# Optimization experiments

Measured on AMD Instinct MI355X. Metric: run time of the kernel, lower is better.

Reference implementation:

```python
import jax, jax.numpy as jnp
import numpy as np
from jax import lax

V, E, H, B, S = 50257, 512, 1024, 128, 256

def setup_inputs() -> dict:
    key = jax.random.key(0)
    k0, k1, k2, k3, k4, k5 = jax.random.split(key, 6)
    scale = 1.0 / np.sqrt(H)  # PyTorch LSTMCell init range ~ U(-1/sqrt(H), 1/sqrt(H))
    return {
        "inputs": jax.random.randint(k0, (B, S), 0, V),
        "embed_table": jax.random.normal(k1, (V, E), dtype=jnp.float32) * 0.02,
        "W_ih": jax.random.uniform(k2, (4 * H, E), dtype=jnp.float32, minval=-scale, maxval=scale),
        "W_hh": jax.random.uniform(k3, (4 * H, H), dtype=jnp.float32, minval=-scale, maxval=scale),
        "b_ih": jax.random.uniform(k4, (4 * H,), dtype=jnp.float32, minval=-scale, maxval=scale),
        "b_hh": jax.random.uniform(k5, (4 * H,), dtype=jnp.float32, minval=-scale, maxval=scale),
    }

def reference(inputs, embed_table, W_ih, W_hh, b_ih, b_hh):
    # Embedding lookup: [B, S, E]
    embeds = embed_table[inputs]
    bias = b_ih + b_hh  # [4H]

    def step(h, x_t):
        # x_t: [B, E], h: [B, H]
        gates = x_t @ W_ih.T + h @ W_hh.T + bias  # [B, 4H]
        i, f, g, o = jnp.split(gates, 4, axis=-1)  # PyTorch gate order: i, f, g, o
        # FAITHFUL to original bug: new cell state is discarded each step, so the
        # carried cell state is always zero -> c_t = sigmoid(i) * tanh(g).
        c_t = jax.nn.sigmoid(i) * jnp.tanh(g)
        h_new = jax.nn.sigmoid(o) * jnp.tanh(c_t)
        return h_new, None

    h0 = jnp.zeros((B, H), dtype=embeds.dtype)
    xs = jnp.swapaxes(embeds, 0, 1)  # [S, B, E]
    h_last, _ = lax.scan(step, h0, xs)
    return h_last  # [B, H]
```

## Files before the change

### kernel.cpp

```cpp
#include <hip/hip_runtime.h>
#include <hip/hip_fp16.h>


typedef __fp16 f16x8 __attribute__((ext_vector_type(8)));
typedef __fp16 f16x4 __attribute__((ext_vector_type(4)));
typedef float  f32x4 __attribute__((ext_vector_type(4)));

#define MFMA16(a, b, c) __builtin_amdgcn_mfma_f32_16x16x32_f16(a, b, c, 0, 0, 0)

__device__ __forceinline__ float sigmoid_f(float x) {
  return 1.f / (1.f + __expf(-x));
}
__device__ __forceinline__ float tanh_f(float x) {
  x = fminf(fmaxf(x, -15.f), 15.f);
  float e = __expf(2.f * x);
  return (e - 1.f) / (e + 1.f);
}

static constexpr int SS = 256;

__global__ void prep_kernel(const float* __restrict__ W_ih, const float* __restrict__ W_hh,
                            const float* __restrict__ b_ih, const float* __restrict__ b_hh,
                            __fp16* __restrict__ Wi3, __fp16* __restrict__ Wh3,
                            float* __restrict__ bias3) {
  int j3 = blockIdx.x;
  int g = j3 >> 10, j = j3 & 1023;
  int orig = (g == 0 ? 0 : (g == 1 ? 2048 : 3072)) + j;
  int tid = threadIdx.x;
  {
    float4 v = *(const float4*)(W_hh + (size_t)orig * 1024 + tid * 4);
    f16x4 o = {(__fp16)v.x, (__fp16)v.y, (__fp16)v.z, (__fp16)v.w};
    *(f16x4*)(Wh3 + (size_t)j3 * 1024 + tid * 4) = o;
  }
  if (tid < 128) {
    float4 v = *(const float4*)(W_ih + (size_t)orig * 512 + tid * 4);
    f16x4 o = {(__fp16)v.x, (__fp16)v.y, (__fp16)v.z, (__fp16)v.w};
    *(f16x4*)(Wi3 + (size_t)j3 * 512 + tid * 4) = o;
  }
  if (tid == 0) bias3[j3] = b_ih[orig] + b_hh[orig];
}

__global__ void gather_kernel(const int* __restrict__ tok, const float* __restrict__ emb,
                              __fp16* __restrict__ X) {
  int m = blockIdx.x;
  int t = m >> 7, b = m & 127;
  int tk = tok[b * SS + t];
  int e0 = threadIdx.x * 8;
  const float* src = emb + (size_t)tk * 512 + e0;
  float4 v0 = *(const float4*)src;
  float4 v1 = *(const float4*)(src + 4);
  f16x8 o;
  o[0] = (__fp16)v0.x; o[1] = (__fp16)v0.y; o[2] = (__fp16)v0.z; o[3] = (__fp16)v0.w;
  o[4] = (__fp16)v1.x; o[5] = (__fp16)v1.y; o[6] = (__fp16)v1.z; o[7] = (__fp16)v1.w;
  *(f16x8*)(X + (size_t)m * 512 + e0) = o;
}

__global__ __launch_bounds__(256, 1) void recur_kernel(const __fp16* __restrict__ Wh3,
                                                       const __fp16* __restrict__ Wi3,
                                                       const __fp16* __restrict__ X,
                                                       const float* __restrict__ bias3,
                                                       __fp16* __restrict__ hbuf,
                                                       int* __restrict__ cnt,
                                                       float* __restrict__ out) {
  const int bid = blockIdx.x;
  const int bg = bid & 7, n = bid >> 3;
  const int b0 = bg * 16, j0 = n * 32;
  const int tid = threadIdx.x, wid = tid >> 6, lane = tid & 63;
  const int l15 = lane & 15, quad = lane >> 4;
  const int kq = wid;
  const int ct_e = wid & 1, rh = wid >> 1;

  __shared__ float gbuf[2][4][3][2][16][20];

  f16x8 wh[3][2][8];
  f16x8 wi[3][2][4];
#pragma unroll
  for (int g = 0; g < 3; ++g)
#pragma unroll
    for (int ct = 0; ct < 2; ++ct) {
      const __fp16* wr = Wh3 + (size_t)(g * 1024 + j0 + ct * 16 + l15) * 1024 + kq * 256 + quad * 8;
#pragma unroll
      for (int kk = 0; kk < 8; ++kk) wh[g][ct][kk] = *(const f16x8*)(wr + kk * 32);
      const __fp16* wr2 = Wi3 + (size_t)(g * 1024 + j0 + ct * 16 + l15) * 512 + kq * 128 + quad * 8;
#pragma unroll
      for (int kk = 0; kk < 4; ++kk) wi[g][ct][kk] = *(const f16x8*)(wr2 + kk * 32);
    }

  float bs[3];
#pragma unroll
  for (int g = 0; g < 3; ++g) bs[g] = bias3[g * 1024 + j0 + ct_e * 16 + l15];

  const __fp16* xrow = X + (size_t)(b0 + l15) * 512 + kq * 128 + quad * 8;
  const __fp16* hrow = hbuf + (size_t)(b0 + l15) * 1024 + kq * 256 + quad * 8;
  int* cbase = cnt + (bg << 8) * 16;

  for (int t = 0; t < SS; ++t) {
    f16x8 xa[4];
    {
      const __fp16* xp = xrow + (size_t)t * 65536;
#pragma unroll
      for (int kk = 0; kk < 4; ++kk) xa[kk] = *(const f16x8*)(xp + kk * 32);
    }
    if (t > 0) {
      const int* pollp = cbase + t * 16;
      for (;;) {
        int v = __hip_atomic_load(pollp, __ATOMIC_RELAXED, __HIP_MEMORY_SCOPE_AGENT);
        if (v >= 32) break;
        __builtin_amdgcn_s_sleep(1);
      }
      asm volatile("" ::: "memory");
    }
    f16x8 ha[8];
    {
      const __fp16* hp = hrow + (size_t)t * 131072;
#pragma unroll
      for (int kk = 0; kk < 8; ++kk) ha[kk] = *(const f16x8*)(hp + kk * 32);
    }
    f32x4 acc[3][2];
#pragma unroll
    for (int g = 0; g < 3; ++g)
#pragma unroll
      for (int ct = 0; ct < 2; ++ct) {
        f32x4 z = {0.f, 0.f, 0.f, 0.f};
        acc[g][ct] = z;
      }
#pragma unroll
    for (int kk = 0; kk < 4; ++kk)
#pragma unroll
      for (int g = 0; g < 3; ++g)
#pragma unroll
        for (int ct = 0; ct < 2; ++ct)
          acc[g][ct] = MFMA16(xa[kk], wi[g][ct][kk], acc[g][ct]);
#pragma unroll
    for (int kk = 0; kk < 8; ++kk)
#pragma unroll
      for (int g = 0; g < 3; ++g)
#pragma unroll
        for (int ct = 0; ct < 2; ++ct)
          acc[g][ct] = MFMA16(ha[kk], wh[g][ct][kk], acc[g][ct]);
    const int tp = t & 1;
#pragma unroll
    for (int g = 0; g < 3; ++g)
#pragma unroll
      for (int ct = 0; ct < 2; ++ct)
#pragma unroll
        for (int r = 0; r < 4; ++r)
          gbuf[tp][kq][g][ct][quad * 4 + r][l15] = acc[g][ct][r];
    __syncthreads();
    float sum[3][2];
#pragma unroll
    for (int g = 0; g < 3; ++g)
#pragma unroll
      for (int rr = 0; rr < 2; ++rr) {
        const int r = rh * 2 + rr;
        sum[g][rr] = gbuf[tp][0][g][ct_e][quad * 4 + r][l15] + gbuf[tp][1][g][ct_e][quad * 4 + r][l15] +
                     gbuf[tp][2][g][ct_e][quad * 4 + r][l15] + gbuf[tp][3][g][ct_e][quad * 4 + r][l15];
      }
#pragma unroll
    for (int rr = 0; rr < 2; ++rr) {
      const int r = rh * 2 + rr;
      float gi = sum[0][rr] + bs[0];
      float gg = sum[1][rr] + bs[1];
      float go = sum[2][rr] + bs[2];
      float cv = sigmoid_f(gi) * tanh_f(gg);
      float hN = sigmoid_f(go) * tanh_f(cv);
      const int row = b0 + quad * 4 + r;
      const int col = j0 + ct_e * 16 + l15;
      if (t == SS - 1) out[(size_t)row * 1024 + col] = hN;
      else hbuf[(size_t)(t + 1) * 131072 + (size_t)row * 1024 + col] = (__fp16)hN;
    }
    if (t < SS - 1) {
      asm volatile("s_waitcnt vmcnt(0)" ::: "memory");
      __syncthreads();
      if (tid == 0)
        __hip_atomic_fetch_add(cbase + (t + 1) * 16, 1,
                               __ATOMIC_RELAXED, __HIP_MEMORY_SCOPE_AGENT);
    }
  }
}

extern "C" void kernel_launch(void* const* d_in, const int* in_sizes, int n_in,
                              void* d_out, int out_size, void* d_ws, size_t ws_size,
                              hipStream_t stream) {
  const int*   tok  = (const int*)d_in[0];
  const float* emb  = (const float*)d_in[1];
  const float* W_ih = (const float*)d_in[2];
  const float* W_hh = (const float*)d_in[3];
  const float* b_ih = (const float*)d_in[4];
  const float* b_hh = (const float*)d_in[5];
  float* out = (float*)d_out;
  char* ws = (char*)d_ws;

  __fp16* X     = (__fp16*)(ws + 0);
  __fp16* Wi3   = (__fp16*)(ws + 33554432);
  __fp16* Wh3   = (__fp16*)(ws + 36700160);
  float*  bias3 = (float*) (ws + 42991616);
  int*    cnt   = (int*)   (ws + 43003904);
  __fp16* hbuf  = (__fp16*)(ws + 43134976);

  (void)hipMemsetAsync(cnt, 0, 131072, stream);
  (void)hipMemsetAsync(hbuf, 0, 131072 * 2, stream);

  prep_kernel<<<3072, 256, 0, stream>>>(W_ih, W_hh, b_ih, b_hh, Wi3, Wh3, bias3);
  gather_kernel<<<32768, 64, 0, stream>>>(tok, emb, X);
  recur_kernel<<<256, 256, 0, stream>>>(Wh3, Wi3, X, bias3, hbuf, cnt, out);
}
```

Before: 1.295 ms.

## Split recurrent blocks across eight waves and prefetch next-step inputs

The recurrent kernel now runs with 512 threads, so each wave handles one column tile and one K-quarter instead of two column tiles. This halves the weight registers per wave and the serial MFMA chain per step. The input projection for step t now runs before the poll on the step's counter, and the next step's embedding slice is loaded before the wait, so both overlap the inter-block synchronisation. In exchange there are more waves per block taking part in each barrier, and register pressure changes under the new launch bounds.

```diff
diff --git a/kernel.cpp b/kernel.cpp
--- a/kernel.cpp
+++ b/kernel.cpp
@@ -55,7 +55,7 @@
   *(f16x8*)(X + (size_t)m * 512 + e0) = o;
 }
 
-__global__ __launch_bounds__(256, 1) void recur_kernel(const __fp16* __restrict__ Wh3,
+__global__ __launch_bounds__(512, 2) void recur_kernel(const __fp16* __restrict__ Wh3,
                                                        const __fp16* __restrict__ Wi3,
                                                        const __fp16* __restrict__ X,
                                                        const float* __restrict__ bias3,
@@ -67,24 +67,23 @@
   const int b0 = bg * 16, j0 = n * 32;
   const int tid = threadIdx.x, wid = tid >> 6, lane = tid & 63;
   const int l15 = lane & 15, quad = lane >> 4;
-  const int kq = wid;
-  const int ct_e = wid & 1, rh = wid >> 1;
+  const int kq = wid >> 1, ct = wid & 1;
+  const int ct_e = wid & 1, rq = wid >> 1;
+  const int lr = lane >> 4;
 
   __shared__ float gbuf[2][4][3][2][16][20];
 
-  f16x8 wh[3][2][8];
-  f16x8 wi[3][2][4];
+  f16x8 wh[3][8];
+  f16x8 wi[3][4];
 #pragma unroll
-  for (int g = 0; g < 3; ++g)
+  for (int g = 0; g < 3; ++g) {
+    const __fp16* wr = Wh3 + (size_t)(g * 1024 + j0 + ct * 16 + l15) * 1024 + kq * 256 + quad * 8;
 #pragma unroll
-    for (int ct = 0; ct < 2; ++ct) {
-      const __fp16* wr = Wh3 + (size_t)(g * 1024 + j0 + ct * 16 + l15) * 1024 + kq * 256 + quad * 8;
+    for (int kk = 0; kk < 8; ++kk) wh[g][kk] = *(const f16x8*)(wr + kk * 32);
+    const __fp16* wr2 = Wi3 + (size_t)(g * 1024 + j0 + ct * 16 + l15) * 512 + kq * 128 + quad * 8;
 #pragma unroll
-      for (int kk = 0; kk < 8; ++kk) wh[g][ct][kk] = *(const f16x8*)(wr + kk * 32);
-      const __fp16* wr2 = Wi3 + (size_t)(g * 1024 + j0 + ct * 16 + l15) * 512 + kq * 128 + quad * 8;
-#pragma unroll
-      for (int kk = 0; kk < 4; ++kk) wi[g][ct][kk] = *(const f16x8*)(wr2 + kk * 32);
-    }
+    for (int kk = 0; kk < 4; ++kk) wi[g][kk] = *(const f16x8*)(wr2 + kk * 32);
+  }
 
   float bs[3];
 #pragma unroll
@@ -92,12 +91,27 @@
 
   const __fp16* xrow = X + (size_t)(b0 + l15) * 512 + kq * 128 + quad * 8;
   const __fp16* hrow = hbuf + (size_t)(b0 + l15) * 1024 + kq * 256 + quad * 8;
-  int* cbase = cnt + (bg << 8) * 16;
+  int* cbase = cnt + bg * (SS * 16);
+
+  f16x8 xa[4];
+#pragma unroll
+  for (int kk = 0; kk < 4; ++kk) xa[kk] = *(const f16x8*)(xrow + kk * 32);
 
   for (int t = 0; t < SS; ++t) {
-    f16x8 xa[4];
+    f32x4 acc[3];
+#pragma unroll
+    for (int g = 0; g < 3; ++g) {
+      f32x4 z = {0.f, 0.f, 0.f, 0.f};
+      acc[g] = z;
+    }
+#pragma unroll
+    for (int kk = 0; kk < 4; ++kk)
+#pragma unroll
+      for (int g = 0; g < 3; ++g)
+        acc[g] = MFMA16(xa[kk], wi[g][kk], acc[g]);
     {
-      const __fp16* xp = xrow + (size_t)t * 65536;
+      const int tn = (t + 1 < SS) ? t + 1 : t;
+      const __fp16* xp = xrow + (size_t)tn * 65536;
 #pragma unroll
       for (int kk = 0; kk < 4; ++kk) xa[kk] = *(const f16x8*)(xp + kk * 32);
     }
@@ -116,55 +130,31 @@
 #pragma unroll
       for (int kk = 0; kk < 8; ++kk) ha[kk] = *(const f16x8*)(hp + kk * 32);
     }
-    f32x4 acc[3][2];
-#pragma unroll
-    for (int g = 0; g < 3; ++g)
-#pragma unroll
-      for (int ct = 0; ct < 2; ++ct) {
-        f32x4 z = {0.f, 0.f, 0.f, 0.f};
-        acc[g][ct] = z;
-      }
-#pragma unroll
-    for (int kk = 0; kk < 4; ++kk)
-#pragma unroll
-      for (int g = 0; g < 3; ++g)
-#pragma unroll
-        for (int ct = 0; ct < 2; ++ct)
-          acc[g][ct] = MFMA16(xa[kk], wi[g][ct][kk], acc[g][ct]);
 #pragma unroll
     for (int kk = 0; kk < 8; ++kk)
 #pragma unroll
       for (int g = 0; g < 3; ++g)
-#pragma unroll
-        for (int ct = 0; ct < 2; ++ct)
-          acc[g][ct] = MFMA16(ha[kk], wh[g][ct][kk], acc[g][ct]);
+        acc[g] = MFMA16(ha[kk], wh[g][kk], acc[g]);
     const int tp = t & 1;
 #pragma unroll
     for (int g = 0; g < 3; ++g)
 #pragma unroll
-      for (int ct = 0; ct < 2; ++ct)
+      for (int r = 0; r < 4; ++r)
+        gbuf[tp][kq][g][ct][quad * 4 + r][l15] = acc[g][r];
+    __syncthreads();
+    {
+      const int row_i = rq * 4 + lr;
+      float s[3];
 #pragma unroll
-        for (int r = 0; r < 4; ++r)
-          gbuf[tp][kq][g][ct][quad * 4 + r][l15] = acc[g][ct][r];
-    __syncthreads();
-    float sum[3][2];
-#pragma unroll
-    for (int g = 0; g < 3; ++g)
-#pragma unroll
-      for (int rr = 0; rr < 2; ++rr) {
-        const int r = rh * 2 + rr;
-        sum[g][rr] = gbuf[tp][0][g][ct_e][quad * 4 + r][l15] + gbuf[tp][1][g][ct_e][quad * 4 + r][l15] +
-                     gbuf[tp][2][g][ct_e][quad * 4 + r][l15] + gbuf[tp][3][g][ct_e][quad * 4 + r][l15];
-      }
-#pragma unroll
-    for (int rr = 0; rr < 2; ++rr) {
-      const int r = rh * 2 + rr;
-      float gi = sum[0][rr] + bs[0];
-      float gg = sum[1][rr] + bs[1];
-      float go = sum[2][rr] + bs[2];
+      for (int g = 0; g < 3; ++g)
+        s[g] = gbuf[tp][0][g][ct_e][row_i][l15] + gbuf[tp][1][g][ct_e][row_i][l15] +
+               gbuf[tp][2][g][ct_e][row_i][l15] + gbuf[tp][3][g][ct_e][row_i][l15];
+      float gi = s[0] + bs[0];
+      float gg = s[1] + bs[1];
+      float go = s[2] + bs[2];
       float cv = sigmoid_f(gi) * tanh_f(gg);
       float hN = sigmoid_f(go) * tanh_f(cv);
-      const int row = b0 + quad * 4 + r;
+      const int row = b0 + row_i;
       const int col = j0 + ct_e * 16 + l15;
       if (t == SS - 1) out[(size_t)row * 1024 + col] = hN;
       else hbuf[(size_t)(t + 1) * 131072 + (size_t)row * 1024 + col] = (__fp16)hN;
@@ -203,5 +193,5 @@
 
   prep_kernel<<<3072, 256, 0, stream>>>(W_ih, W_hh, b_ih, b_hh, Wi3, Wh3, bias3);
   gather_kernel<<<32768, 64, 0, stream>>>(tok, emb, X);
-  recur_kernel<<<256, 256, 0, stream>>>(Wh3, Wi3, X, bias3, hbuf, cnt, out);
+  recur_kernel<<<256, 512, 0, stream>>>(Wh3, Wi3, X, bias3, hbuf, cnt, out);
 }
```

Result: faster. 1.235 ms (-4.6%).
